# Kernel optimization log

Measured on AMD Instinct MI355X. Metric: run time of the kernel, lower is better.

## Reference

```python
import jax, jax.numpy as jnp
import numpy as np

ALPHA = 0.9  # init alpha, adj='DAD'


def setup_inputs() -> dict:
    key = jax.random.key(0)
    k1, k2, k3, k4 = jax.random.split(key, 4)
    N, C, E = 100000, 64, 3200000
    labels = jax.random.uniform(k1, (N, C), dtype=jnp.float32)
    mask = jax.random.randint(k2, (N,), 0, 2).astype(bool)
    src = jax.random.randint(k3, (E,), 0, N, dtype=jnp.int64)
    dst = jax.random.randint(k4, (E,), 0, N, dtype=jnp.int64)
    return {"labels": labels, "mask": mask, "src": src, "dst": dst, "num_layers": 10}


def reference(labels, mask, src, dst, num_layers):
    N = labels.shape[0]
    # mask: y = zeros; y[mask] = labels[mask]
    y0 = jnp.where(mask[:, None], labels, jnp.zeros((), labels.dtype))
    last = (1.0 - ALPHA) * y0  # confidence = 1
    # in-degrees via scatter-count at dst, clamped to >= 1
    degs = jax.ops.segment_sum(jnp.ones(dst.shape, labels.dtype), dst, num_segments=N)
    degs = jnp.maximum(degs, 1.0)
    norm = (degs ** -0.5)[:, None]  # DAD: D^-1/2 on both sides

    def step(y, _):
        y = norm * y                                   # left D^-1/2
        h = jax.ops.segment_sum(y[src], dst, num_segments=N)  # A @ y (copy_u + sum)
        y = ALPHA * h * norm                           # right D^-1/2
        y = jnp.clip(last + y, 0.0, 1.0)               # post_step clamp
        return y, None

    y, _ = jax.lax.scan(step, y0, None, length=num_layers)
    return y
```

## Files before the change

kernel.cpp:

```cpp
#include <hip/hip_runtime.h>
#include <hip/hip_fp16.h>


#define ALPHA 0.9f
#define C 64
#define BSHIFT 9
#define NCHUNK 256


__global__ void chunk_hist_kernel(const int* __restrict__ dst, int* __restrict__ cnt,
                                  int E, int epc) {
    __shared__ int h[256];
    h[threadIdx.x] = 0;
    __syncthreads();
    int c = blockIdx.x;
    int e1 = min(c * epc + epc, E);
    for (int e = c * epc + threadIdx.x; e < e1; e += 256) {
        int d = __builtin_nontemporal_load(&dst[e]);
        atomicAdd(&h[d >> BSHIFT], 1);
    }
    __syncthreads();
    cnt[c * 256 + threadIdx.x] = h[threadIdx.x];
}

__global__ void bucket_scan_kernel(int* __restrict__ cnt, int* __restrict__ bucket_base,
                                   int* __restrict__ row_ptr, int N, int E) {
    __shared__ int tmp[256];
    int b = threadIdx.x;
    int s = 0;
    for (int c = 0; c < NCHUNK; ++c) {
        int t = cnt[c * 256 + b];
        cnt[c * 256 + b] = s;
        s += t;
    }
    tmp[b] = s;
    __syncthreads();
    int v = s;
    for (int off = 1; off < 256; off <<= 1) {
        int add = (b >= off) ? tmp[b - off] : 0;
        __syncthreads();
        tmp[b] += add;
        __syncthreads();
    }
    bucket_base[b] = tmp[b] - v;
    if (b == 255) { bucket_base[256] = tmp[255]; row_ptr[N] = E; }
}

__global__ void bucket_scatter_kernel(const int* __restrict__ src, const int* __restrict__ dst,
                                      const int* __restrict__ cnt,
                                      const int* __restrict__ bucket_base,
                                      unsigned* __restrict__ tmp, int E, int epc) {
    __shared__ int cur[256];
    int c = blockIdx.x;
    cur[threadIdx.x] = bucket_base[threadIdx.x] + cnt[c * 256 + threadIdx.x];
    __syncthreads();
    int e1 = min(c * epc + epc, E);
    for (int e = c * epc + threadIdx.x; e < e1; e += 256) {
        int d = __builtin_nontemporal_load(&dst[e]);
        int s = __builtin_nontemporal_load(&src[e]);
        int pos = atomicAdd(&cur[d >> BSHIFT], 1);
        tmp[pos] = ((unsigned)(d & 511) << 23) | (unsigned)s;
    }
}

__global__ void bucket_sort_kernel(const unsigned* __restrict__ tmp,
                                   const int* __restrict__ bucket_base,
                                   int* __restrict__ row_ptr,
                                   float* __restrict__ norm,
                                   int* __restrict__ col, int N) {
    __shared__ int ldeg[512];
    __shared__ int lexc[512];
    __shared__ int lcur[512];
    __shared__ int stmp[256];
    int b = blockIdx.x;
    int lo = b << BSHIFT;
    int nn = min(512, N - lo);
    int ebeg = bucket_base[b];
    int eend = bucket_base[b + 1];
    int t = threadIdx.x;
    ldeg[t] = 0; ldeg[t + 256] = 0;
    __syncthreads();
    for (int e = ebeg + t; e < eend; e += 256) {
        atomicAdd(&ldeg[tmp[e] >> 23], 1);
    }
    __syncthreads();
    int d0 = ldeg[2 * t], d1 = ldeg[2 * t + 1];
    int p = d0 + d1;
    stmp[t] = p;
    __syncthreads();
    for (int off = 1; off < 256; off <<= 1) {
        int add = (t >= off) ? stmp[t - off] : 0;
        __syncthreads();
        stmp[t] += add;
        __syncthreads();
    }
    int excp = stmp[t] - p;
    lexc[2 * t] = excp;
    lexc[2 * t + 1] = excp + d0;
    __syncthreads();
    for (int i = t; i < nn; i += 256) {
        int rp = ebeg + lexc[i];
        row_ptr[lo + i] = rp;
        lcur[i] = rp;
        norm[lo + i] = rsqrtf(fmaxf((float)ldeg[i], 1.0f));
    }
    __syncthreads();
    for (int e = ebeg + t; e < eend; e += 256) {
        unsigned pk = tmp[e];
        int pos = atomicAdd(&lcur[pk >> 23], 1);
        col[pos] = (int)(pk & 0x7FFFFFu);
    }
}


__global__ void init_z_kernel(const float* __restrict__ labels,
                              const int* __restrict__ mask,
                              const float* __restrict__ norm,
                              __half* __restrict__ z, int total8 ) {
    int i = blockIdx.x * blockDim.x + threadIdx.x;
    if (i >= total8) return;
    int row = i >> 3;
    float4 a = ((const float4*)labels)[i * 2];
    float4 b = ((const float4*)labels)[i * 2 + 1];
    float m = (mask[row] != 0) ? norm[row] : 0.0f;
    __half2 h[4];
    h[0] = __floats2half2_rn(m * a.x, m * a.y);
    h[1] = __floats2half2_rn(m * a.z, m * a.w);
    h[2] = __floats2half2_rn(m * b.x, m * b.y);
    h[3] = __floats2half2_rn(m * b.z, m * b.w);
    ((float4*)z)[i] = *(const float4*)h;
}

template <bool OUT_FP32>
__global__ void prop_kernel(const __half* __restrict__ z_old,
                            void* __restrict__ z_new_v,
                            const int* __restrict__ row_ptr,
                            const int* __restrict__ col,
                            const float* __restrict__ norm,
                            const float* __restrict__ labels,
                            const int* __restrict__ mask, int N) {
    int gtid = blockIdx.x * blockDim.x + threadIdx.x;
    int node = gtid >> 6;
    if (node >= N) return;
    int lane = threadIdx.x & 63;
    int sub = lane >> 3;
    int ch8 = lane & 7;

    int beg = row_ptr[node];
    int end = row_ptr[node + 1];
    int deg = end - beg;

    float acc[8];
#pragma unroll
    for (int k = 0; k < 8; ++k) acc[k] = 0.0f;

    if (deg > 0) {
        int base = beg + sub;
        int last = end - 1;
        int T = (deg + 7) >> 3;
        int Tpad = (T + 3) & ~3;

        float n0, n1, n2, n3;
        float4 r0, r1, r2, r3;

#define FETCH(t, nv, rv)                                                      \
        do {                                                                  \
            int pp = base + ((t) << 3);                                       \
            int pcl = pp < last ? pp : last;                                  \
            int sv = col[pcl];                                                \
            nv = (pp < end) ? 1.0f : 0.0f;                                    \
            rv = ((const float4*)(z_old + (size_t)sv * C))[ch8];              \
        } while (0)

#define CONSUME(nv, rv)                                                       \
        do {                                                                  \
            const __half* hh = (const __half*)&rv;                            \
            acc[0] = fmaf(__half2float(hh[0]), nv, acc[0]);                   \
            acc[1] = fmaf(__half2float(hh[1]), nv, acc[1]);                   \
            acc[2] = fmaf(__half2float(hh[2]), nv, acc[2]);                   \
            acc[3] = fmaf(__half2float(hh[3]), nv, acc[3]);                   \
            acc[4] = fmaf(__half2float(hh[4]), nv, acc[4]);                   \
            acc[5] = fmaf(__half2float(hh[5]), nv, acc[5]);                   \
            acc[6] = fmaf(__half2float(hh[6]), nv, acc[6]);                   \
            acc[7] = fmaf(__half2float(hh[7]), nv, acc[7]);                   \
        } while (0)

        FETCH(0, n0, r0);
        FETCH(1, n1, r1);
        FETCH(2, n2, r2);
        FETCH(3, n3, r3);
        for (int t = 4; t < Tpad; t += 4) {
            CONSUME(n0, r0); FETCH(t + 0, n0, r0);
            CONSUME(n1, r1); FETCH(t + 1, n1, r1);
            CONSUME(n2, r2); FETCH(t + 2, n2, r2);
            CONSUME(n3, r3); FETCH(t + 3, n3, r3);
        }
        CONSUME(n0, r0);
        CONSUME(n1, r1);
        CONSUME(n2, r2);
        CONSUME(n3, r3);
#undef FETCH
#undef CONSUME
    }

#pragma unroll
    for (int k = 0; k < 8; ++k) {
        acc[k] += __shfl_xor(acc[k], 8, 64);
        acc[k] += __shfl_xor(acc[k], 16, 64);
        acc[k] += __shfl_xor(acc[k], 32, 64);
    }

    if (sub == 0) {
        float nr = norm[node];
        float m = (mask[node] != 0) ? (1.0f - ALPHA) : 0.0f;
        const float* lrow = labels + (size_t)node * C + ch8 * 8;
        float4 la = ((const float4*)lrow)[0];
        float4 lb = ((const float4*)lrow)[1];
        float o[8];
        o[0] = fminf(fmaxf(m * la.x + ALPHA * nr * acc[0], 0.0f), 1.0f);
        o[1] = fminf(fmaxf(m * la.y + ALPHA * nr * acc[1], 0.0f), 1.0f);
        o[2] = fminf(fmaxf(m * la.z + ALPHA * nr * acc[2], 0.0f), 1.0f);
        o[3] = fminf(fmaxf(m * la.w + ALPHA * nr * acc[3], 0.0f), 1.0f);
        o[4] = fminf(fmaxf(m * lb.x + ALPHA * nr * acc[4], 0.0f), 1.0f);
        o[5] = fminf(fmaxf(m * lb.y + ALPHA * nr * acc[5], 0.0f), 1.0f);
        o[6] = fminf(fmaxf(m * lb.z + ALPHA * nr * acc[6], 0.0f), 1.0f);
        o[7] = fminf(fmaxf(m * lb.w + ALPHA * nr * acc[7], 0.0f), 1.0f);
        if (OUT_FP32) {
            float* orow = (float*)z_new_v + (size_t)node * C + ch8 * 8;
            float4 v0; v0.x = o[0]; v0.y = o[1]; v0.z = o[2]; v0.w = o[3];
            float4 v1; v1.x = o[4]; v1.y = o[5]; v1.z = o[6]; v1.w = o[7];
            ((float4*)orow)[0] = v0;
            ((float4*)orow)[1] = v1;
        } else {
            __half2 h[4];
            h[0] = __floats2half2_rn(nr * o[0], nr * o[1]);
            h[1] = __floats2half2_rn(nr * o[2], nr * o[3]);
            h[2] = __floats2half2_rn(nr * o[4], nr * o[5]);
            h[3] = __floats2half2_rn(nr * o[6], nr * o[7]);
            __half* orow = (__half*)z_new_v + (size_t)node * C + ch8 * 8;
            *(float4*)orow = *(const float4*)h;
        }
    }
}


__global__ void zero_f32_kernel(float* __restrict__ p, int n) {
    int i = blockIdx.x * blockDim.x + threadIdx.x;
    if (i < n) p[i] = 0.0f;
}
__global__ void deg_count_f_kernel(const int* __restrict__ dst, float* __restrict__ deg, int E) {
    int i = blockIdx.x * blockDim.x + threadIdx.x;
    if (i < E) atomicAdd(&deg[dst[i]], 1.0f);
}
__global__ void make_norm_f_kernel(float* __restrict__ deg, int N) {
    int i = blockIdx.x * blockDim.x + threadIdx.x;
    if (i < N) deg[i] = rsqrtf(fmaxf(deg[i], 1.0f));
}
__global__ void init_yh_kernel(const float* __restrict__ labels, const int* __restrict__ mask,
                               float* __restrict__ y, float* __restrict__ h, int total4) {
    int i = blockIdx.x * blockDim.x + threadIdx.x;
    if (i >= total4) return;
    int row = i >> 4;
    float4 lv = ((const float4*)labels)[i];
    float m = (mask[row] != 0) ? 1.0f : 0.0f;
    float4 yv; yv.x = m * lv.x; yv.y = m * lv.y; yv.z = m * lv.z; yv.w = m * lv.w;
    ((float4*)y)[i] = yv;
    float4 z; z.x = 0.f; z.y = 0.f; z.z = 0.f; z.w = 0.f;
    ((float4*)h)[i] = z;
}
__global__ void scatter_kernel(const float* __restrict__ y, const int* __restrict__ src,
                               const int* __restrict__ dst, const float* __restrict__ norm,
                               float* __restrict__ h, int E) {
    int gtid = blockIdx.x * blockDim.x + threadIdx.x;
    int e = gtid >> 6;
    int lane = threadIdx.x & 63;
    if (e >= E) return;
    int s = src[e]; int d = dst[e];
    float v = y[(size_t)s * C + lane] * norm[s];
    atomicAdd(&h[(size_t)d * C + lane], v);
}
__global__ void finalize_kernel(const float* __restrict__ labels, const int* __restrict__ mask,
                                const float* __restrict__ norm, float* __restrict__ h,
                                float* __restrict__ y, int total4) {
    int i = blockIdx.x * blockDim.x + threadIdx.x;
    if (i >= total4) return;
    int row = i >> 4;
    float4 hv = ((float4*)h)[i];
    float4 lv = ((const float4*)labels)[i];
    float m = (mask[row] != 0) ? (1.0f - ALPHA) : 0.0f;
    float nr = norm[row];
    float4 o;
    o.x = fminf(fmaxf(m * lv.x + ALPHA * hv.x * nr, 0.0f), 1.0f);
    o.y = fminf(fmaxf(m * lv.y + ALPHA * hv.y * nr, 0.0f), 1.0f);
    o.z = fminf(fmaxf(m * lv.z + ALPHA * hv.z * nr, 0.0f), 1.0f);
    o.w = fminf(fmaxf(m * lv.w + ALPHA * hv.w * nr, 0.0f), 1.0f);
    ((float4*)y)[i] = o;
    float4 z; z.x = 0.f; z.y = 0.f; z.z = 0.f; z.w = 0.f;
    ((float4*)h)[i] = z;
}


extern "C" void kernel_launch(void* const* d_in, const int* in_sizes, int n_in,
                              void* d_out, int out_size, void* d_ws, size_t ws_size,
                              hipStream_t stream) {
    const float* labels = (const float*)d_in[0];
    const int*   mask   = (const int*)d_in[1];
    const int*   src    = (const int*)d_in[2];
    const int*   dst    = (const int*)d_in[3];

    const int N = in_sizes[1];
    const int E = in_sizes[2];
    const int num_layers = 10;
    const int B = 256;

    size_t fixed_ints = (size_t)257 + (size_t)NCHUNK * 256 + (N + 1) + N + E;
    size_t ybytes = (size_t)N * C * 2;
    size_t tmpbytes = (size_t)E * 4;
    size_t tailbytes = (ybytes > tmpbytes ? ybytes : tmpbytes) + ybytes;
    size_t need = fixed_ints * 4 + 256 + tailbytes;
    bool pack_ok = (N < (1 << 23));

    if (ws_size >= need && pack_ok) {
        char* w = (char*)d_ws;
        int*   bucket_base = (int*)w;             w += 257 * 4;
        int*   cnt         = (int*)w;             w += (size_t)NCHUNK * 256 * 4;
        int*   row_ptr     = (int*)w;             w += (size_t)(N + 1) * 4;
        float* norm        = (float*)w;           w += (size_t)N * 4;
        int*   col         = (int*)w;             w += (size_t)E * 4;
        w = (char*)(((uintptr_t)w + 255) & ~(uintptr_t)255);
        __half* zA         = (__half*)w;          w += ybytes;
        __half* zB         = (__half*)w;
        unsigned* tmp      = (unsigned*)zB;

        int epc = (E + NCHUNK - 1) / NCHUNK;
        int NB = (N + 511) >> BSHIFT;

        chunk_hist_kernel<<<NCHUNK, 256, 0, stream>>>(dst, cnt, E, epc);
        bucket_scan_kernel<<<1, 256, 0, stream>>>(cnt, bucket_base, row_ptr, N, E);
        bucket_scatter_kernel<<<NCHUNK, 256, 0, stream>>>(src, dst, cnt, bucket_base,
                                                          tmp, E, epc);
        bucket_sort_kernel<<<NB, 256, 0, stream>>>(tmp, bucket_base, row_ptr,
                                                   norm, col, N);

        int total8 = N * C / 8;
        init_z_kernel<<<(total8 + B - 1) / B, B, 0, stream>>>(labels, mask, norm,
                                                              zA, total8);
        const int prop_blocks = (int)(((size_t)N * 64 + B - 1) / B);
        for (int l = 0; l < num_layers - 1; ++l) {
            __half* zi = (l & 1) ? zB : zA;
            __half* zo = (l & 1) ? zA : zB;
            prop_kernel<false><<<prop_blocks, B, 0, stream>>>(zi, zo, row_ptr, col,
                                                              norm, labels, mask, N);
        }
        prop_kernel<true><<<prop_blocks, B, 0, stream>>>(zB, d_out, row_ptr, col,
                                                         norm, labels, mask, N);
    } else {
        const int total4 = N * C / 4;
        float* y = (float*)d_out;
        float* wsf = (float*)d_ws;
        float* norm = wsf;
        float* h = wsf + ((N + 15) & ~15);
        zero_f32_kernel<<<(N + B - 1) / B, B, 0, stream>>>(norm, N);
        deg_count_f_kernel<<<(E + B - 1) / B, B, 0, stream>>>(dst, norm, E);
        make_norm_f_kernel<<<(N + B - 1) / B, B, 0, stream>>>(norm, N);
        init_yh_kernel<<<(total4 + B - 1) / B, B, 0, stream>>>(labels, mask, y, h, total4);
        const int scatter_blocks = (int)(((size_t)E * C + B - 1) / B);
        for (int l = 0; l < num_layers; ++l) {
            scatter_kernel<<<scatter_blocks, B, 0, stream>>>(y, src, dst, norm, h, E);
            finalize_kernel<<<(total4 + B - 1) / B, B, 0, stream>>>(labels, mask, norm,
                                                                    h, y, total4);
        }
    }
}
```

Before: 756.6 us.

## Map two nodes per wavefront, deepen gather pipeline, precompute fp16 label term

Each 64-lane wavefront now handles two nodes, with four edge slots per node instead of eight, so lanes idle less on low-degree nodes. The gather loop keeps eight fetches in flight instead of four and handles the remainder explicitly. A precomputed fp16 (1-alpha)*masked-labels buffer replaces the per-layer fp32 label and mask reads in the epilogue when workspace allows. The cost is more registers (lower occupancy), divergence when the paired nodes have different degrees, an extra workspace buffer, and fp16 rounding of the label term.

```diff
diff --git a/kernel.cpp b/kernel.cpp
--- a/kernel.cpp
+++ b/kernel.cpp
@@ -116,19 +116,31 @@
 __global__ void init_z_kernel(const float* __restrict__ labels,
                               const int* __restrict__ mask,
                               const float* __restrict__ norm,
-                              __half* __restrict__ z, int total8 ) {
+                              __half* __restrict__ z,
+                              __half* __restrict__ last16,
+                              int total8 ) {
     int i = blockIdx.x * blockDim.x + threadIdx.x;
     if (i >= total8) return;
     int row = i >> 3;
     float4 a = ((const float4*)labels)[i * 2];
     float4 b = ((const float4*)labels)[i * 2 + 1];
-    float m = (mask[row] != 0) ? norm[row] : 0.0f;
+    bool mk = mask[row] != 0;
+    float m = mk ? norm[row] : 0.0f;
     __half2 h[4];
     h[0] = __floats2half2_rn(m * a.x, m * a.y);
     h[1] = __floats2half2_rn(m * a.z, m * a.w);
     h[2] = __floats2half2_rn(m * b.x, m * b.y);
     h[3] = __floats2half2_rn(m * b.z, m * b.w);
     ((float4*)z)[i] = *(const float4*)h;
+    if (last16) {
+        float ml = mk ? (1.0f - ALPHA) : 0.0f;
+        __half2 g[4];
+        g[0] = __floats2half2_rn(ml * a.x, ml * a.y);
+        g[1] = __floats2half2_rn(ml * a.z, ml * a.w);
+        g[2] = __floats2half2_rn(ml * b.x, ml * b.y);
+        g[3] = __floats2half2_rn(ml * b.z, ml * b.w);
+        ((float4*)last16)[i] = *(const float4*)g;
+    }
 }
 
 template <bool OUT_FP32>
@@ -137,36 +149,38 @@
                             const int* __restrict__ row_ptr,
                             const int* __restrict__ col,
                             const float* __restrict__ norm,
+                            const __half* __restrict__ last16,
                             const float* __restrict__ labels,
                             const int* __restrict__ mask, int N) {
     int gtid = blockIdx.x * blockDim.x + threadIdx.x;
-    int node = gtid >> 6;
-    if (node >= N) return;
+    int wid = gtid >> 6;
     int lane = threadIdx.x & 63;
-    int sub = lane >> 3;
+    int node = (wid << 1) + (lane >> 5);
+    int sub = (lane >> 3) & 3;
     int ch8 = lane & 7;
 
-    int beg = row_ptr[node];
-    int end = row_ptr[node + 1];
+    bool ok = node < N;
+    int beg = 0, end = 0;
+    if (ok) { beg = row_ptr[node]; end = row_ptr[node + 1]; }
     int deg = end - beg;
+    int lastc = max(end - 1, 0);
+    int Tl = (deg + 3) >> 2;
+    int T = max(Tl, __shfl_xor(Tl, 32, 64));
 
     float acc[8];
 #pragma unroll
     for (int k = 0; k < 8; ++k) acc[k] = 0.0f;
 
-    if (deg > 0) {
+    if (T > 0) {
         int base = beg + sub;
-        int last = end - 1;
-        int T = (deg + 7) >> 3;
-        int Tpad = (T + 3) & ~3;
-
-        float n0, n1, n2, n3;
-        float4 r0, r1, r2, r3;
+
+        float n0, n1, n2, n3, n4, n5, n6, n7;
+        float4 r0, r1, r2, r3, r4, r5, r6, r7;
 
 #define FETCH(t, nv, rv)                                                      \
         do {                                                                  \
-            int pp = base + ((t) << 3);                                       \
-            int pcl = pp < last ? pp : last;                                  \
+            int pp = base + ((t) << 2);                                       \
+            int pcl = min(pp, lastc);                                         \
             int sv = col[pcl];                                                \
             nv = (pp < end) ? 1.0f : 0.0f;                                    \
             rv = ((const float4*)(z_old + (size_t)sv * C))[ch8];              \
@@ -185,20 +199,29 @@
             acc[7] = fmaf(__half2float(hh[7]), nv, acc[7]);                   \
         } while (0)
 
-        FETCH(0, n0, r0);
-        FETCH(1, n1, r1);
-        FETCH(2, n2, r2);
-        FETCH(3, n3, r3);
-        for (int t = 4; t < Tpad; t += 4) {
+        FETCH(0, n0, r0); FETCH(1, n1, r1); FETCH(2, n2, r2); FETCH(3, n3, r3);
+        FETCH(4, n4, r4); FETCH(5, n5, r5); FETCH(6, n6, r6); FETCH(7, n7, r7);
+        int t = 8;
+        for (; t + 8 <= T; t += 8) {
             CONSUME(n0, r0); FETCH(t + 0, n0, r0);
             CONSUME(n1, r1); FETCH(t + 1, n1, r1);
             CONSUME(n2, r2); FETCH(t + 2, n2, r2);
             CONSUME(n3, r3); FETCH(t + 3, n3, r3);
+            CONSUME(n4, r4); FETCH(t + 4, n4, r4);
+            CONSUME(n5, r5); FETCH(t + 5, n5, r5);
+            CONSUME(n6, r6); FETCH(t + 6, n6, r6);
+            CONSUME(n7, r7); FETCH(t + 7, n7, r7);
         }
-        CONSUME(n0, r0);
-        CONSUME(n1, r1);
-        CONSUME(n2, r2);
-        CONSUME(n3, r3);
+        int rr = T - t;
+        if (rr > 0) { CONSUME(n0, r0); FETCH(t + 0, n0, r0); }
+        if (rr > 1) { CONSUME(n1, r1); FETCH(t + 1, n1, r1); }
+        if (rr > 2) { CONSUME(n2, r2); FETCH(t + 2, n2, r2); }
+        if (rr > 3) { CONSUME(n3, r3); FETCH(t + 3, n3, r3); }
+        if (rr > 4) { CONSUME(n4, r4); FETCH(t + 4, n4, r4); }
+        if (rr > 5) { CONSUME(n5, r5); FETCH(t + 5, n5, r5); }
+        if (rr > 6) { CONSUME(n6, r6); FETCH(t + 6, n6, r6); }
+        CONSUME(n0, r0); CONSUME(n1, r1); CONSUME(n2, r2); CONSUME(n3, r3);
+        CONSUME(n4, r4); CONSUME(n5, r5); CONSUME(n6, r6); CONSUME(n7, r7);
 #undef FETCH
 #undef CONSUME
     }
@@ -207,24 +230,29 @@
     for (int k = 0; k < 8; ++k) {
         acc[k] += __shfl_xor(acc[k], 8, 64);
         acc[k] += __shfl_xor(acc[k], 16, 64);
-        acc[k] += __shfl_xor(acc[k], 32, 64);
-    }
-
-    if (sub == 0) {
+    }
+
+    if (sub == 0 && ok) {
         float nr = norm[node];
-        float m = (mask[node] != 0) ? (1.0f - ALPHA) : 0.0f;
-        const float* lrow = labels + (size_t)node * C + ch8 * 8;
-        float4 la = ((const float4*)lrow)[0];
-        float4 lb = ((const float4*)lrow)[1];
+        float anr = ALPHA * nr;
+        float la[8];
+        if (last16) {
+            float4 lv = ((const float4*)(last16 + (size_t)node * C))[ch8];
+            const __half* lh = (const __half*)&lv;
+#pragma unroll
+            for (int k = 0; k < 8; ++k) la[k] = __half2float(lh[k]);
+        } else {
+            const float* lrow = labels + (size_t)node * C + ch8 * 8;
+            float4 A = ((const float4*)lrow)[0];
+            float4 Bv = ((const float4*)lrow)[1];
+            float m = (mask[node] != 0) ? (1.0f - ALPHA) : 0.0f;
+            la[0] = m * A.x;  la[1] = m * A.y;  la[2] = m * A.z;  la[3] = m * A.w;
+            la[4] = m * Bv.x; la[5] = m * Bv.y; la[6] = m * Bv.z; la[7] = m * Bv.w;
+        }
         float o[8];
-        o[0] = fminf(fmaxf(m * la.x + ALPHA * nr * acc[0], 0.0f), 1.0f);
-        o[1] = fminf(fmaxf(m * la.y + ALPHA * nr * acc[1], 0.0f), 1.0f);
-        o[2] = fminf(fmaxf(m * la.z + ALPHA * nr * acc[2], 0.0f), 1.0f);
-        o[3] = fminf(fmaxf(m * la.w + ALPHA * nr * acc[3], 0.0f), 1.0f);
-        o[4] = fminf(fmaxf(m * lb.x + ALPHA * nr * acc[4], 0.0f), 1.0f);
-        o[5] = fminf(fmaxf(m * lb.y + ALPHA * nr * acc[5], 0.0f), 1.0f);
-        o[6] = fminf(fmaxf(m * lb.z + ALPHA * nr * acc[6], 0.0f), 1.0f);
-        o[7] = fminf(fmaxf(m * lb.w + ALPHA * nr * acc[7], 0.0f), 1.0f);
+#pragma unroll
+        for (int k = 0; k < 8; ++k)
+            o[k] = fminf(fmaxf(la[k] + anr * acc[k], 0.0f), 1.0f);
         if (OUT_FP32) {
             float* orow = (float*)z_new_v + (size_t)node * C + ch8 * 8;
             float4 v0; v0.x = o[0]; v0.y = o[1]; v0.z = o[2]; v0.w = o[3];
@@ -316,11 +344,12 @@
     size_t fixed_ints = (size_t)257 + (size_t)NCHUNK * 256 + (N + 1) + N + E;
     size_t ybytes = (size_t)N * C * 2;
     size_t tmpbytes = (size_t)E * 4;
-    size_t tailbytes = (ybytes > tmpbytes ? ybytes : tmpbytes) + ybytes;
-    size_t need = fixed_ints * 4 + 256 + tailbytes;
+    size_t span = (tmpbytes > ybytes ? tmpbytes : ybytes);
+    size_t need_base = fixed_ints * 4 + 256 + ybytes + span;
+    size_t need_l16  = need_base + ybytes;
     bool pack_ok = (N < (1 << 23));
 
-    if (ws_size >= need && pack_ok) {
+    if (ws_size >= need_base && pack_ok) {
         char* w = (char*)d_ws;
         int*   bucket_base = (int*)w;             w += 257 * 4;
         int*   cnt         = (int*)w;             w += (size_t)NCHUNK * 256 * 4;
@@ -331,6 +360,7 @@
         __half* zA         = (__half*)w;          w += ybytes;
         __half* zB         = (__half*)w;
         unsigned* tmp      = (unsigned*)zB;
+        __half* last16     = (ws_size >= need_l16) ? (__half*)(w + span) : nullptr;
 
         int epc = (E + NCHUNK - 1) / NCHUNK;
         int NB = (N + 511) >> BSHIFT;
@@ -344,16 +374,19 @@
 
         int total8 = N * C / 8;
         init_z_kernel<<<(total8 + B - 1) / B, B, 0, stream>>>(labels, mask, norm,
-                                                              zA, total8);
-        const int prop_blocks = (int)(((size_t)N * 64 + B - 1) / B);
+                                                              zA, last16, total8);
+        const int nwaves = (N + 1) >> 1;
+        const int prop_blocks = (int)(((size_t)nwaves * 64 + B - 1) / B);
         for (int l = 0; l < num_layers - 1; ++l) {
             __half* zi = (l & 1) ? zB : zA;
             __half* zo = (l & 1) ? zA : zB;
             prop_kernel<false><<<prop_blocks, B, 0, stream>>>(zi, zo, row_ptr, col,
-                                                              norm, labels, mask, N);
+                                                              norm, last16,
+                                                              labels, mask, N);
         }
         prop_kernel<true><<<prop_blocks, B, 0, stream>>>(zB, d_out, row_ptr, col,
-                                                         norm, labels, mask, N);
+                                                         norm, last16,
+                                                         labels, mask, N);
     } else {
         const int total4 = N * C / 4;
         float* y = (float*)d_out;
```

Result: no change. 751.3 us (-0.7%).
